# Kernel tuning notes

Hardware: AMD Instinct MI355X
Metric: run time of the kernel (lower is better)

## Reference

```python
import jax, jax.numpy as jnp
import numpy as np

BS, N, XC, K, YS = 64, 1024, 1024, 256, 768

def setup_inputs() -> dict:
    key = jax.random.key(0)
    ks = jax.random.split(key, 5)
    return {
        "x": jax.random.normal(ks[0], (BS, N, XC), dtype=jnp.float32),
        "y": jax.random.normal(ks[1], (BS, YS), dtype=jnp.float32),
        "W_ch": jax.random.normal(ks[2], (K, XC), dtype=jnp.float32) * 0.02,
        "b_ch": jax.random.normal(ks[3], (K,), dtype=jnp.float32) * 0.02,
        "W_y": jax.random.normal(ks[4], (K, YS), dtype=jnp.float32) * 0.02,
    }

def reference(x, y, W_ch, b_ch, W_y):
    # y_k: [bs, k] (no bias)
    y_k = jnp.einsum('bs,ks->bk', y, W_y)
    # channel affine on every spatial position, batched: [bs, n, k]
    x_k = jnp.einsum('bnc,kc->bnk', x, W_ch) + b_ch
    # add per-sample y_k (broadcast over spatial dim), tanh, softmax over k
    z = jnp.tanh(x_k + y_k[:, None, :])
    attn = jax.nn.softmax(z, axis=-1)
    # torch.cat over dim=0 of per-sample [n, k] blocks -> [bs*n, k]
    return attn.reshape(-1, attn.shape[-1])
```

## Files before the change

kernel.cpp:

```cpp
#include <hip/hip_runtime.h>


#define XC    1024
#define KOUT  256
#define NT    16
#define LDSZ  16384

typedef float        f32x4_t  __attribute__((ext_vector_type(4)));
typedef unsigned int u32x4_t  __attribute__((ext_vector_type(4)));
typedef unsigned int u32x2_t  __attribute__((ext_vector_type(2)));
typedef __bf16       bf16x8_t __attribute__((ext_vector_type(8)));

__device__ __forceinline__ unsigned short f2bf(float f) {
  unsigned int u = __float_as_uint(f);
  u += 0x7fffu + ((u >> 16) & 1u);
  return (unsigned short)(u >> 16);
}

__device__ __forceinline__ unsigned int pack2bf(float a, float b) {
  unsigned int ua = __float_as_uint(a) + 0x8000u;
  unsigned int ub = __float_as_uint(b) + 0x8000u;
  return (ua >> 16) | (ub & 0xffff0000u);
}

__device__ __forceinline__ float fast_tanh(float v) {
  float e = __expf(2.0f * v);
  return 1.0f - 2.0f / (e + 1.0f);
}

#define LGKM_BARRIER() do {                                  \
    asm volatile("s_waitcnt lgkmcnt(0)" ::: "memory");       \
    __builtin_amdgcn_s_barrier();                            \
    __builtin_amdgcn_sched_barrier(0);                       \
  } while (0)

__global__ void prep_kernel(const float* __restrict__ Wch,
                            const float* __restrict__ y,
                            const float* __restrict__ Wy,
                            const float* __restrict__ bch,
                            unsigned short* __restrict__ wbf,
                            float* __restrict__ biasws) {
  if (blockIdx.x < 256) {
    const int k = blockIdx.x;
    const int u = threadIdx.x;
    f32x4_t v = ((const f32x4_t*)(Wch + k * XC))[u];
    const int c0   = u << 2;
    const int t    = c0 >> 6;
    const int ch   = (c0 & 63) >> 3;
    const int kk   = ch >> 2;
    const int lg   = ch & 3;
    const int half = (c0 >> 2) & 1;
    const int wv   = k >> 6;
    const int ni   = (k >> 4) & 3;
    const int lr   = k & 15;
    const int lane = (lg << 4) | lr;
    unsigned int lo = (unsigned int)f2bf(v.x) | ((unsigned int)f2bf(v.y) << 16);
    unsigned int hi = (unsigned int)f2bf(v.z) | ((unsigned int)f2bf(v.w) << 16);
    char* p = (char*)wbf +
              ((size_t)((((t << 2) + wv) * 2 + kk) * 4 + ni) << 10) +
              (lane << 4) + (half << 3);
    *(u32x2_t*)p = (u32x2_t){lo, hi};
  } else {
    __shared__ __align__(16) float ys[768];
    const int b = blockIdx.x - 256;
    const int k = threadIdx.x;
    for (int i = k; i < 768; i += 256) ys[i] = y[b * 768 + i];
    __syncthreads();
    const f32x4_t* w4 = (const f32x4_t*)(Wy + k * 768);
    const f32x4_t* y4 = (const f32x4_t*)ys;
    float s = 0.f;
#pragma unroll 8
    for (int i = 0; i < 192; ++i) {
      f32x4_t w = w4[i], a = y4[i];
      s = fmaf(w.x, a.x, s); s = fmaf(w.y, a.y, s);
      s = fmaf(w.z, a.z, s); s = fmaf(w.w, a.w, s);
    }
    biasws[b * 256 + k] = s + bch[k];
  }
}

__global__ __launch_bounds__(256, 2) void fused_kernel(
    const float* __restrict__ x, const unsigned short* __restrict__ wbf,
    const float* __restrict__ bias, float* __restrict__ out) {
  __shared__ __align__(16) unsigned char smem[LDSZ];
  const int tid = threadIdx.x;
  const int l   = tid & 63;
  const int wv  = tid >> 6;
  const int lr  = l & 15;
  const int lg  = l >> 4;
  const int m0  = blockIdx.x << 6;
  const int bidx = m0 >> 10;
  const int rr  = tid >> 4;
  const int c4  = tid & 15;
  const int t0  = blockIdx.x & 15;

  f32x4_t acc[4][4];
#pragma unroll
  for (int i = 0; i < 4; ++i)
#pragma unroll
    for (int j = 0; j < 4; ++j) acc[i][j] = (f32x4_t){0.f, 0.f, 0.f, 0.f};

  const float* xb = x + (size_t)m0 * XC + (size_t)rr * XC + (c4 << 2);
  const char* wsrc = (const char*)wbf + (wv << 13) + (l << 4);
  f32x4_t av0[4], av1[4], av2[4];
  bf16x8_t bfrA[8], bfrB[8];

#define LOADA(dst, tt) do {                                                  \
    _Pragma("unroll")                                                        \
    for (int j = 0; j < 4; ++j)                                              \
      dst[j] = *(const f32x4_t*)(xb + (size_t)(j << 4) * XC + ((tt) << 6));  \
  } while (0)

#define LOADB(dst, tt) do {                                                  \
    const char* g = wsrc + (size_t)(tt) * 32768;                             \
    _Pragma("unroll")                                                        \
    for (int f = 0; f < 8; ++f)                                              \
      dst[f] = __builtin_bit_cast(bf16x8_t, *(const u32x4_t*)(g + (f << 10)));\
  } while (0)

#define WRITEA(src, buf) do {                                                \
    _Pragma("unroll")                                                        \
    for (int j = 0; j < 4; ++j) {                                            \
      const int row = (j << 4) + rr;                                         \
      unsigned int lo = pack2bf(src[j].x, src[j].y);                         \
      unsigned int hi = pack2bf(src[j].z, src[j].w);                         \
      char* p = (char*)smem + ((buf) << 13) + row * 128 +                    \
                (((c4 >> 1) ^ (row & 7)) << 4) + ((c4 & 1) << 3);            \
      *(u32x2_t*)p = (u32x2_t){lo, hi};                                      \
    }                                                                        \
  } while (0)

#define COMPUTE(buf, bsrc) do {                                              \
    const u32x4_t* aB = (const u32x4_t*)(smem + ((buf) << 13));              \
    _Pragma("unroll")                                                        \
    for (int kk = 0; kk < 2; ++kk) {                                         \
      const int cs = ((kk << 2) | lg) ^ (lr & 7);                            \
      bf16x8_t afr[4];                                                       \
      _Pragma("unroll")                                                      \
      for (int mi = 0; mi < 4; ++mi)                                         \
        afr[mi] = __builtin_bit_cast(bf16x8_t, aB[(((mi << 4) + lr) << 3) + cs]);\
      _Pragma("unroll")                                                      \
      for (int mi = 0; mi < 4; ++mi)                                         \
        _Pragma("unroll")                                                    \
        for (int nj = 0; nj < 4; ++nj)                                       \
          acc[mi][nj] = __builtin_amdgcn_mfma_f32_16x16x32_bf16(             \
              afr[mi], bsrc[(kk << 2) | nj], acc[mi][nj], 0, 0, 0);          \
    }                                                                        \
  } while (0)

#define STEP(s, bC, bN, aW, aL) do {                                         \
    if ((s) + 1 < NT) LOADB(bN, (((s) + 1 + t0) & 15));                      \
    if ((s) + 3 < NT) LOADA(aL, (((s) + 3 + t0) & 15));                      \
    COMPUTE((s) & 1, bC);                                                    \
    if ((s) + 1 < NT) { WRITEA(aW, ((s) + 1) & 1); LGKM_BARRIER(); }         \
  } while (0)

  LOADB(bfrA, t0);
  LOADA(av0, t0);
  LOADA(av1, (t0 + 1) & 15);
  LOADA(av2, (t0 + 2) & 15);
  WRITEA(av0, 0);
  LGKM_BARRIER();

  STEP( 0, bfrA, bfrB, av1, av0);
  STEP( 1, bfrB, bfrA, av2, av1);
  STEP( 2, bfrA, bfrB, av0, av2);
  STEP( 3, bfrB, bfrA, av1, av0);
  STEP( 4, bfrA, bfrB, av2, av1);
  STEP( 5, bfrB, bfrA, av0, av2);
  STEP( 6, bfrA, bfrB, av1, av0);
  STEP( 7, bfrB, bfrA, av2, av1);
  STEP( 8, bfrA, bfrB, av0, av2);
  STEP( 9, bfrB, bfrA, av1, av0);
  STEP(10, bfrA, bfrB, av2, av1);
  STEP(11, bfrB, bfrA, av0, av2);
  STEP(12, bfrA, bfrB, av1, av0);
  STEP(13, bfrB, bfrA, av2, av1);
  STEP(14, bfrA, bfrB, av0, av2);
  STEP(15, bfrB, bfrA, av1, av0);

  __syncthreads();

#undef LOADA
#undef LOADB
#undef WRITEA
#undef COMPUTE
#undef STEP

  float* wred    = (float*)smem;
  float* rowstat = (float*)(smem + 1024);

  float brow[4];
#pragma unroll
  for (int ni = 0; ni < 4; ++ni)
    brow[ni] = bias[(bidx << 8) + (wv << 6) + (ni << 4) + lr];

#pragma unroll
  for (int mi = 0; mi < 4; ++mi)
#pragma unroll
    for (int ni = 0; ni < 4; ++ni)
#pragma unroll
      for (int r = 0; r < 4; ++r)
        acc[mi][ni][r] = fast_tanh(acc[mi][ni][r] + brow[ni]);

#pragma unroll
  for (int mi = 0; mi < 4; ++mi)
#pragma unroll
    for (int r = 0; r < 4; ++r) {
      float m = fmaxf(fmaxf(acc[mi][0][r], acc[mi][1][r]),
                      fmaxf(acc[mi][2][r], acc[mi][3][r]));
      m = fmaxf(m, __shfl_xor(m, 1));
      m = fmaxf(m, __shfl_xor(m, 2));
      m = fmaxf(m, __shfl_xor(m, 4));
      m = fmaxf(m, __shfl_xor(m, 8));
      if (lr == 0) wred[(wv << 6) + (mi << 4) + (lg << 2) + r] = m;
    }
  __syncthreads();
  if (tid < 64)
    rowstat[tid] = fmaxf(fmaxf(wred[tid], wred[64 + tid]),
                         fmaxf(wred[128 + tid], wred[192 + tid]));
  __syncthreads();

#pragma unroll
  for (int mi = 0; mi < 4; ++mi)
#pragma unroll
    for (int r = 0; r < 4; ++r) {
      const int row = (mi << 4) + (lg << 2) + r;
      const float m = rowstat[row];
      float s = 0.f;
#pragma unroll
      for (int ni = 0; ni < 4; ++ni) {
        float e = __expf(acc[mi][ni][r] - m);
        acc[mi][ni][r] = e;
        s += e;
      }
      s += __shfl_xor(s, 1);
      s += __shfl_xor(s, 2);
      s += __shfl_xor(s, 4);
      s += __shfl_xor(s, 8);
      if (lr == 0) wred[(wv << 6) + row] = s;
    }
  __syncthreads();
  if (tid < 64)
    rowstat[tid] = 1.0f / (wred[tid] + wred[64 + tid] +
                           wred[128 + tid] + wred[192 + tid]);
  __syncthreads();

#pragma unroll
  for (int mi = 0; mi < 4; ++mi)
#pragma unroll
    for (int r = 0; r < 4; ++r) {
      const int row = (mi << 4) + (lg << 2) + r;
      const float rinv = rowstat[row];
      float* orow = out + (size_t)(m0 + row) * KOUT + (wv << 6) + lr;
#pragma unroll
      for (int ni = 0; ni < 4; ++ni)
        orow[ni << 4] = acc[mi][ni][r] * rinv;
    }
}

extern "C" void kernel_launch(void* const* d_in, const int* in_sizes, int n_in,
                              void* d_out, int out_size, void* d_ws, size_t ws_size,
                              hipStream_t stream) {
  (void)in_sizes; (void)n_in; (void)out_size; (void)ws_size;
  const float* x   = (const float*)d_in[0];
  const float* y   = (const float*)d_in[1];
  const float* Wch = (const float*)d_in[2];
  const float* bch = (const float*)d_in[3];
  const float* Wy  = (const float*)d_in[4];
  float* out = (float*)d_out;
  unsigned short* wbf = (unsigned short*)d_ws;
  float* biasws = (float*)((char*)d_ws + 512 * 1024);

  hipLaunchKernelGGL(prep_kernel, dim3(320), dim3(256), 0, stream,
                     Wch, y, Wy, bch, wbf, biasws);
  hipLaunchKernelGGL(fused_kernel, dim3(1024), dim3(256), 0, stream,
                     x, wbf, biasws, out);
}
```

Measured before the change: 111.1 us.

## Shrink prefetch register buffers to allow three waves per SIMD

Cuts the main GEMM pipeline from double-buffered B fragments and triple-buffered A prefetch to a single B buffer and double-buffered A. B for the next tile is now loaded after the MFMAs of the current tile instead of before. The launch bound rises from 2 to 3 blocks per CU so that the lower register use buys more occupancy to hide latency. In exchange, each wave has less software prefetch depth, and the B loads are exposed at the start of each step.

```diff
diff --git a/kernel.cpp b/kernel.cpp
--- a/kernel.cpp
+++ b/kernel.cpp
@@ -79,7 +79,7 @@
   }
 }
 
-__global__ __launch_bounds__(256, 2) void fused_kernel(
+__global__ __launch_bounds__(256, 3) void fused_kernel(
     const float* __restrict__ x, const unsigned short* __restrict__ wbf,
     const float* __restrict__ bias, float* __restrict__ out) {
   __shared__ __align__(16) unsigned char smem[LDSZ];
@@ -102,8 +102,8 @@
 
   const float* xb = x + (size_t)m0 * XC + (size_t)rr * XC + (c4 << 2);
   const char* wsrc = (const char*)wbf + (wv << 13) + (l << 4);
-  f32x4_t av0[4], av1[4], av2[4];
-  bf16x8_t bfrA[8], bfrB[8];
+  f32x4_t av0[4], av1[4];
+  bf16x8_t bfr[8];
 
 #define LOADA(dst, tt) do {                                                  \
     _Pragma("unroll")                                                        \
@@ -111,11 +111,11 @@
       dst[j] = *(const f32x4_t*)(xb + (size_t)(j << 4) * XC + ((tt) << 6));  \
   } while (0)
 
-#define LOADB(dst, tt) do {                                                  \
+#define LOADB(tt) do {                                                       \
     const char* g = wsrc + (size_t)(tt) * 32768;                             \
     _Pragma("unroll")                                                        \
     for (int f = 0; f < 8; ++f)                                              \
-      dst[f] = __builtin_bit_cast(bf16x8_t, *(const u32x4_t*)(g + (f << 10)));\
+      bfr[f] = __builtin_bit_cast(bf16x8_t, *(const u32x4_t*)(g + (f << 10)));\
   } while (0)
 
 #define WRITEA(src, buf) do {                                                \
@@ -130,7 +130,7 @@
     }                                                                        \
   } while (0)
 
-#define COMPUTE(buf, bsrc) do {                                              \
+#define COMPUTE(buf) do {                                                    \
     const u32x4_t* aB = (const u32x4_t*)(smem + ((buf) << 13));              \
     _Pragma("unroll")                                                        \
     for (int kk = 0; kk < 2; ++kk) {                                         \
@@ -144,40 +144,39 @@
         _Pragma("unroll")                                                    \
         for (int nj = 0; nj < 4; ++nj)                                       \
           acc[mi][nj] = __builtin_amdgcn_mfma_f32_16x16x32_bf16(             \
-              afr[mi], bsrc[(kk << 2) | nj], acc[mi][nj], 0, 0, 0);          \
+              afr[mi], bfr[(kk << 2) | nj], acc[mi][nj], 0, 0, 0);           \
     }                                                                        \
   } while (0)
 
-#define STEP(s, bC, bN, aW, aL) do {                                         \
-    if ((s) + 1 < NT) LOADB(bN, (((s) + 1 + t0) & 15));                      \
-    if ((s) + 3 < NT) LOADA(aL, (((s) + 3 + t0) & 15));                      \
-    COMPUTE((s) & 1, bC);                                                    \
-    if ((s) + 1 < NT) { WRITEA(aW, ((s) + 1) & 1); LGKM_BARRIER(); }         \
-  } while (0)
-
-  LOADB(bfrA, t0);
+#define STEP(s, aCur, aNext) do {                                            \
+    COMPUTE((s) & 1);                                                        \
+    if ((s) + 1 < NT) LOADB((((s) + 1 + t0) & 15));                          \
+    if ((s) + 2 < NT) LOADA(aCur, (((s) + 2 + t0) & 15));                    \
+    if ((s) + 1 < NT) { WRITEA(aNext, ((s) + 1) & 1); LGKM_BARRIER(); }      \
+  } while (0)
+
+  LOADB(t0);
   LOADA(av0, t0);
   LOADA(av1, (t0 + 1) & 15);
-  LOADA(av2, (t0 + 2) & 15);
   WRITEA(av0, 0);
   LGKM_BARRIER();
 
-  STEP( 0, bfrA, bfrB, av1, av0);
-  STEP( 1, bfrB, bfrA, av2, av1);
-  STEP( 2, bfrA, bfrB, av0, av2);
-  STEP( 3, bfrB, bfrA, av1, av0);
-  STEP( 4, bfrA, bfrB, av2, av1);
-  STEP( 5, bfrB, bfrA, av0, av2);
-  STEP( 6, bfrA, bfrB, av1, av0);
-  STEP( 7, bfrB, bfrA, av2, av1);
-  STEP( 8, bfrA, bfrB, av0, av2);
-  STEP( 9, bfrB, bfrA, av1, av0);
-  STEP(10, bfrA, bfrB, av2, av1);
-  STEP(11, bfrB, bfrA, av0, av2);
-  STEP(12, bfrA, bfrB, av1, av0);
-  STEP(13, bfrB, bfrA, av2, av1);
-  STEP(14, bfrA, bfrB, av0, av2);
-  STEP(15, bfrB, bfrA, av1, av0);
+  STEP( 0, av0, av1);
+  STEP( 1, av1, av0);
+  STEP( 2, av0, av1);
+  STEP( 3, av1, av0);
+  STEP( 4, av0, av1);
+  STEP( 5, av1, av0);
+  STEP( 6, av0, av1);
+  STEP( 7, av1, av0);
+  STEP( 8, av0, av1);
+  STEP( 9, av1, av0);
+  STEP(10, av0, av1);
+  STEP(11, av1, av0);
+  STEP(12, av0, av1);
+  STEP(13, av1, av0);
+  STEP(14, av0, av1);
+  STEP(15, av1, av0);
 
   __syncthreads();
 
```

New measurement: 121.9 us. +9.7%, slower.
